# Kernel optimization log

Hardware: AMD Instinct MI355X
Metric: run time of the kernel (lower is better)

Reference implementation:

```python
import jax, jax.numpy as jnp
import numpy as np
from jax import lax

IMPOSSIBLE = -10000.0
B, T, N = 64, 2048, 128


def setup_inputs() -> dict:
    key = jax.random.key(0)
    ks = jax.random.split(key, 8)
    emissions = jax.random.normal(ks[0], (B, T, N), dtype=jnp.float32)
    mask = jnp.ones((B, T), dtype=bool)
    target = jax.random.bernoulli(ks[1], 0.5, (B, T, N))
    transitions = jax.random.normal(ks[2], (N, N), dtype=jnp.float32) * 0.1
    start_transitions = jax.random.normal(ks[3], (N,), dtype=jnp.float32) * 0.1
    end_transitions = jax.random.normal(ks[4], (N,), dtype=jnp.float32) * 0.1
    forbidden_transitions = jax.random.bernoulli(ks[5], 0.2, (N, N))
    start_forbidden_transitions = jax.random.bernoulli(ks[6], 0.2, (N,))
    end_forbidden_transitions = jax.random.bernoulli(ks[7], 0.2, (N,))
    return {
        "emissions": emissions,
        "mask": mask,
        "target": target,
        "transitions": transitions,
        "start_transitions": start_transitions,
        "end_transitions": end_transitions,
        "forbidden_transitions": forbidden_transitions,
        "start_forbidden_transitions": start_forbidden_transitions,
        "end_forbidden_transitions": end_forbidden_transitions,
    }


def reference(emissions, mask, target, transitions, start_transitions,
              end_transitions, forbidden_transitions,
              start_forbidden_transitions, end_forbidden_transitions):
    # Apply hard constraints
    trans = jnp.where(forbidden_transitions, IMPOSSIBLE, transitions)        # [N,N]
    st = jnp.where(start_forbidden_transitions, IMPOSSIBLE, start_transitions)  # [N]
    en = jnp.where(end_forbidden_transitions, IMPOSSIBLE, end_transitions)      # [N]

    # Channel 0: supervised (emissions clamped to target set), channel 1: full partition
    sup_em = jnp.where(target, emissions, IMPOSSIBLE)
    bi = jnp.stack([sup_em, emissions], axis=0)            # [2,B,T,N]
    bi = jnp.moveaxis(bi, 2, 0)                            # [T,2,B,N]

    alpha0 = bi[0] + st                                    # [2,B,N]

    def step(alpha, em_t):
        # alpha: [2,B,N]; logsumexp over previous tag i of alpha_i + trans_ij
        new = jax.nn.logsumexp(alpha[..., :, None] + trans[None, None], axis=-2) + em_t
        return new, new

    _, rest = lax.scan(step, alpha0, bi[1:])               # rest: [T-1,2,B,N]
    outs = jnp.concatenate([alpha0[None], rest], axis=0)   # [T,2,B,N]

    lengths = mask.astype(jnp.int32).sum(-1) - 1           # [B]
    last_out = outs[lengths, :, jnp.arange(B)] + en        # [B,2,N]
    z = jax.nn.logsumexp(last_out, axis=-1)                # [B,2]
    return -(z[:, 0] - z[:, 1])                            # [B] loss per sample
```

## Files before the change

### kernel.cpp

```cpp
#include <hip/hip_runtime.h>
#include <cstdint>
#include <cstddef>

#define IMPOSSIBLE -10000.0f
#define INV_LN2 1.44269504088896340736f
#define LN2 0.69314718055994530942f

constexpr int B = 64;
constexpr int T = 2048;
constexpr int N = 128;
constexpr int WSLOT = 132;

typedef _Float16 h2 __attribute__((ext_vector_type(2)));
typedef _Float16 h8 __attribute__((ext_vector_type(8)));

typedef __attribute__((address_space(3))) uint32_t lds_u32_t;
typedef __attribute__((address_space(1))) const uint32_t g_u32_t;

__device__ __forceinline__ void gload_lds4(const void* g, void* l) {
    __builtin_amdgcn_global_load_lds((g_u32_t*)g, (lds_u32_t*)l, 4, 0, 0);
}

struct SmemT {
    __align__(16) _Float16 p_buf[2][128];
    __align__(16) float ring_em[9][128];
    __align__(16) int ring_tg[9][128];
    float wred[4];
};

template<bool FWD, bool SUP, bool FM>
__device__ __forceinline__ void run_chain(
    SmemT& sm,
    const float* __restrict__ embase,
    const int* __restrict__ tgbase,
    const float* __restrict__ transitions,
    const int* __restrict__ forb,
    const float* __restrict__ bnd_tr,
    const int* __restrict__ bnd_forb,
    const int tlast_rt,
    float* __restrict__ wsl)
{
    const int tid = (int)threadIdx.x;
    const int wave = tid >> 6;
    const int lane = tid & 63;
    const int h = lane >> 5;
    const int j = (wave << 5) | (lane & 31);

    const int tlast = FM ? (T - 1) : tlast_rt;
    const int mid = tlast >> 1;
    const int nsteps = FWD ? mid : (tlast - mid);

    h2 e2[32];
    #pragma unroll
    for (int k = 0; k < 8; ++k) {
        const int cch = ((lane & 7) + k) & 7;
        const int ib = (h << 6) + (cch << 3);
        #pragma unroll
        for (int m = 0; m < 4; ++m) {
            const int i0 = ib + (m << 1);
            const int idx0 = FWD ? (i0 * N + j) : (j * N + i0);
            const int idx1 = FWD ? ((i0 + 1) * N + j) : (j * N + i0 + 1);
            const float f0 = forb[idx0] ? 0.0f : __expf(transitions[idx0]);
            const float f1 = forb[idx1] ? 0.0f : __expf(transitions[idx1]);
            e2[(k << 2) + m] = h2{(_Float16)f0, (_Float16)f1};
        }
    }

    const float bnd = bnd_forb[j] ? IMPOSSIBLE : bnd_tr[j];
    const int r0 = FWD ? 0 : tlast;
    const float em0 = embase[(size_t)r0 * N + j];
    const int tg0 = SUP ? tgbase[(size_t)r0 * N + j] : 1;
    const float v0l = ((tg0 ? em0 : IMPOSSIBLE) + bnd) * INV_LN2;

    float mx = v0l;
    #pragma unroll
    for (int d = 1; d < 64; d <<= 1) mx = fmaxf(mx, __shfl_xor(mx, d));
    if (lane == 0) sm.wred[wave] = mx;
    __syncthreads();
    mx = fmaxf(fmaxf(sm.wred[0], sm.wred[1]), fmaxf(sm.wred[2], sm.wred[3]));

    float Mtot = rintf(mx);
    const float p0 = exp2f(v0l - Mtot);
    if (h == 0) sm.p_buf[0][j] = (_Float16)p0;

    float svE = FWD ? p0 : __expf(bnd);
    float svM = FWD ? Mtot : 0.0f;

    if (wave == 0) {
        #pragma unroll
        for (int s = 1; s <= 8; ++s) {
            int srow, drow;
            if (FWD) {
                srow = s; drow = s & 7;
            } else {
                const int r = tlast - s;
                const int ok = FM ? 1 : (r >= 0);
                srow = ok ? r : 0;
                drow = ok ? (r & 7) : 8;
            }
            const float* gse = embase + (size_t)srow * N + lane;
            gload_lds4(gse, &sm.ring_em[drow][0]);
            gload_lds4(gse + 64, &sm.ring_em[drow][64]);
            if (SUP) {
                const int* gst = tgbase + (size_t)srow * N + lane;
                gload_lds4(gst, &sm.ring_tg[drow][0]);
                gload_lds4(gst + 64, &sm.ring_tg[drow][64]);
            }
        }
        if (SUP) asm volatile("s_waitcnt vmcnt(24)" ::: "memory");
        else     asm volatile("s_waitcnt vmcnt(12)" ::: "memory");
    }
    __syncthreads();

    float fx;
    {
        const int t1 = FWD ? 1 : (tlast - 1);
        const int rr = t1 & 7;
        const float em_n = sm.ring_em[rr][j];
        if (SUP) {
            const int tg_n = sm.ring_tg[rr][j];
            fx = tg_n ? __expf(em_n) : 0.0f;
        } else {
            fx = __expf(em_n);
        }
    }

    const _Float16* pb0 = &sm.p_buf[0][h << 6];
    const _Float16* pb1 = &sm.p_buf[1][h << 6];
    const h2 one2 = h2{(_Float16)1.0f, (_Float16)1.0f};

    #pragma unroll 2
    for (int it = 0; it < nsteps; ++it) {
        const int t = FWD ? (1 + it) : (tlast - 1 - it);

        asm volatile("s_waitcnt lgkmcnt(0)\n\ts_barrier" ::: "memory");

        if (wave == 0) {
            int srow, drow;
            if (FWD) {
                srow = t + 8; drow = srow & 7;
            } else {
                const int tt = t - 8;
                const int ok = (tt >= 0);
                srow = ok ? tt : 0;
                drow = ok ? (tt & 7) : 8;
            }
            const float* gse = embase + (size_t)srow * N + lane;
            gload_lds4(gse, &sm.ring_em[drow][0]);
            gload_lds4(gse + 64, &sm.ring_em[drow][64]);
            if (SUP) {
                const int* gst = tgbase + (size_t)srow * N + lane;
                gload_lds4(gst, &sm.ring_tg[drow][0]);
                gload_lds4(gst + 64, &sm.ring_tg[drow][64]);
            }
        }

        const int cur = (it & 1) ^ 1;
        const _Float16* pbase = (cur ^ 1) ? pb1 : pb0;

        h8 pvv[8];
        #pragma unroll
        for (int k = 0; k < 8; ++k) {
            const int cch = ((lane & 7) + k) & 7;
            pvv[k] = *reinterpret_cast<const h8*>(pbase + (cch << 3));
        }

        float acc0 = 0.f, acc1 = 0.f, acc2 = 0.f, acc3 = 0.f;
        float ps0 = 0.f, ps1 = 0.f, ps2 = 0.f, ps3 = 0.f;
        #pragma unroll
        for (int k = 0; k < 8; ++k) {
            const h8 pv = pvv[k];
            const h2 w0 = __builtin_shufflevector(pv, pv, 0, 1);
            const h2 w1 = __builtin_shufflevector(pv, pv, 2, 3);
            const h2 w2 = __builtin_shufflevector(pv, pv, 4, 5);
            const h2 w3 = __builtin_shufflevector(pv, pv, 6, 7);
            acc0 = __builtin_amdgcn_fdot2(w0, e2[(k << 2) + 0], acc0, false);
            acc1 = __builtin_amdgcn_fdot2(w1, e2[(k << 2) + 1], acc1, false);
            acc2 = __builtin_amdgcn_fdot2(w2, e2[(k << 2) + 2], acc2, false);
            acc3 = __builtin_amdgcn_fdot2(w3, e2[(k << 2) + 3], acc3, false);
            ps0 = __builtin_amdgcn_fdot2(w0, one2, ps0, false);
            ps1 = __builtin_amdgcn_fdot2(w1, one2, ps1, false);
            ps2 = __builtin_amdgcn_fdot2(w2, one2, ps2, false);
            ps3 = __builtin_amdgcn_fdot2(w3, one2, ps3, false);
        }
        const float s = (acc0 + acc1) + (acc2 + acc3);
        const float ph = (ps0 + ps1) + (ps2 + ps3);

        float x = s, y = s;
        asm volatile("v_permlane32_swap_b32 %0, %1" : "+v"(x), "+v"(y));
        const float stot = x + y;
        float u = ph, v = ph;
        asm volatile("v_permlane32_swap_b32 %0, %1" : "+v"(u), "+v"(v));
        const float psum = fmaxf(u + v, 1e-30f);

        const float sc = __builtin_amdgcn_rcpf(psum);
        Mtot += __log2f(psum);

        const float na = stot * (fx * sc);
        if (t == mid) {
            svE = FWD ? na : (stot * sc);
            svM = Mtot;
        }

        if (h == 0) sm.p_buf[cur][j] = (_Float16)na;

        {
            const int nt = FWD ? (t + 1) : (t - 1);
            const int rr = nt & 7;
            const float em_n = sm.ring_em[rr][j];
            if (SUP) {
                const int tg_n = sm.ring_tg[rr][j];
                fx = tg_n ? __expf(em_n) : 0.0f;
            } else {
                fx = __expf(em_n);
            }
        }

        if (wave == 0) {
            if (SUP) asm volatile("s_waitcnt vmcnt(24)" ::: "memory");
            else     asm volatile("s_waitcnt vmcnt(12)" ::: "memory");
        }
    }

    if (h == 0) wsl[j] = svE;
    if (tid == 0) wsl[128] = svM;
}

__global__ __launch_bounds__(256, 1) void crf_chain_kernel(
    const float* __restrict__ emissions,
    const int* __restrict__ mask,
    const int* __restrict__ target,
    const float* __restrict__ transitions,
    const float* __restrict__ start_tr,
    const float* __restrict__ end_tr,
    const int* __restrict__ forb,
    const int* __restrict__ start_forb,
    const int* __restrict__ end_forb,
    float* __restrict__ ws)
{
    __shared__ SmemT sm;
    __shared__ int lred[4];

    const int dir = (int)blockIdx.x >> 7;
    const int chain = (int)blockIdx.x & 127;
    const int c = chain >> 6;
    const int b = chain & 63;
    const int tid = (int)threadIdx.x;
    const int wave = tid >> 6;
    const int lane = tid & 63;

    int lsum = 0;
    for (int k = tid; k < T; k += 256) lsum += (mask[b * T + k] != 0);
    #pragma unroll
    for (int d = 1; d < 64; d <<= 1) lsum += __shfl_xor(lsum, d);
    if (lane == 0) lred[wave] = lsum;
    __syncthreads();
    const int tlast = (lred[0] + lred[1] + lred[2] + lred[3]) - 1;
    const bool fm = (tlast == T - 1);

    const float* embase = emissions + (size_t)b * T * N;
    const int* tgbase = target + (size_t)b * T * N;
    float* wsl = ws + (size_t)(dir * 128 + chain) * WSLOT;

    if (dir == 0) {
        if (c == 0) {
            if (fm) run_chain<true, true, true>(sm, embase, tgbase, transitions, forb, start_tr, start_forb, tlast, wsl);
            else    run_chain<true, true, false>(sm, embase, tgbase, transitions, forb, start_tr, start_forb, tlast, wsl);
        } else {
            if (fm) run_chain<true, false, true>(sm, embase, tgbase, transitions, forb, start_tr, start_forb, tlast, wsl);
            else    run_chain<true, false, false>(sm, embase, tgbase, transitions, forb, start_tr, start_forb, tlast, wsl);
        }
    } else {
        if (c == 0) {
            if (fm) run_chain<false, true, true>(sm, embase, tgbase, transitions, forb, end_tr, end_forb, tlast, wsl);
            else    run_chain<false, true, false>(sm, embase, tgbase, transitions, forb, end_tr, end_forb, tlast, wsl);
        } else {
            if (fm) run_chain<false, false, true>(sm, embase, tgbase, transitions, forb, end_tr, end_forb, tlast, wsl);
            else    run_chain<false, false, false>(sm, embase, tgbase, transitions, forb, end_tr, end_forb, tlast, wsl);
        }
    }
}

__global__ void crf_dot_kernel(const float* __restrict__ ws,
                               float* __restrict__ out) {
    const int b = (int)blockIdx.x;
    const int tid = (int)threadIdx.x;
    const int w = tid >> 6;
    const int lane = tid & 63;
    const int chain = w * 64 + b;

    const float* fv = ws + (size_t)chain * WSLOT;
    const float* bv = ws + (size_t)(128 + chain) * WSLOT;

    float term = fv[lane] * bv[lane] + fv[lane + 64] * bv[lane + 64];
    #pragma unroll
    for (int d = 1; d < 64; d <<= 1) term += __shfl_xor(term, d);

    __shared__ float zz[2];
    if (lane == 0) zz[w] = LN2 * (fv[128] + bv[128]) + __logf(term);
    __syncthreads();
    if (tid == 0) out[b] = zz[1] - zz[0];
}

extern "C" void kernel_launch(void* const* d_in, const int* in_sizes, int n_in,
                              void* d_out, int out_size, void* d_ws, size_t ws_size,
                              hipStream_t stream) {
    const float* emissions = (const float*)d_in[0];
    const int* mask = (const int*)d_in[1];
    const int* target = (const int*)d_in[2];
    const float* transitions = (const float*)d_in[3];
    const float* start_tr = (const float*)d_in[4];
    const float* end_tr = (const float*)d_in[5];
    const int* forb = (const int*)d_in[6];
    const int* start_forb = (const int*)d_in[7];
    const int* end_forb = (const int*)d_in[8];
    float* out = (float*)d_out;
    float* ws = (float*)d_ws;

    crf_chain_kernel<<<dim3(4 * B), dim3(256), 0, stream>>>(
        emissions, mask, target, transitions, start_tr, end_tr,
        forb, start_forb, end_forb, ws);
    crf_dot_kernel<<<dim3(B), dim3(128), 0, stream>>>(ws, out);
}
```

Baseline: 453.8 us.

## Pack four CRF chains per 1024-thread block sharing a common step loop

Merges four independent 256-thread chain workgroups into one 1024-thread block with per-group shared memory, launching 64 blocks instead of 256. Every group iterates to the block-wide maximum step count, skipping work when inactive. The s_barrier inside the loop now synchronises all 16 waves, so each chain step waits on the slowest of four chains. This trades per-step barrier cost for fewer blocks, which may fit better on the CUs.

After: 1.039 ms. 129% more time.

```diff
diff --git a/kernel.cpp b/kernel.cpp
--- a/kernel.cpp
+++ b/kernel.cpp
@@ -10,6 +10,7 @@
 constexpr int T = 2048;
 constexpr int N = 128;
 constexpr int WSLOT = 132;
+constexpr int GROUPS = 4;
 
 typedef _Float16 h2 __attribute__((ext_vector_type(2)));
 typedef _Float16 h8 __attribute__((ext_vector_type(8)));
@@ -26,6 +27,8 @@
     __align__(16) float ring_em[9][128];
     __align__(16) int ring_tg[9][128];
     float wred[4];
+    int lred[4];
+    int nred;
 };
 
 template<bool FWD, bool SUP, bool FM>
@@ -38,17 +41,21 @@
     const float* __restrict__ bnd_tr,
     const int* __restrict__ bnd_forb,
     const int tlast_rt,
+    const int nrun_rt,
     float* __restrict__ wsl)
 {
     const int tid = (int)threadIdx.x;
-    const int wave = tid >> 6;
+    const int gtid = tid & 255;
+    const int gwave = gtid >> 6;
     const int lane = tid & 63;
     const int h = lane >> 5;
-    const int j = (wave << 5) | (lane & 31);
+    const int j = (gwave << 5) | (lane & 31);
 
     const int tlast = FM ? (T - 1) : tlast_rt;
     const int mid = tlast >> 1;
-    const int nsteps = FWD ? mid : (tlast - mid);
+    const int nself = FWD ? mid : (tlast - mid);
+    const int nrun = FM ? (FWD ? ((T - 1) >> 1) : (T - 1 - ((T - 1) >> 1)))
+                        : nrun_rt;
 
     h2 e2[32];
     #pragma unroll
@@ -75,7 +82,7 @@
     float mx = v0l;
     #pragma unroll
     for (int d = 1; d < 64; d <<= 1) mx = fmaxf(mx, __shfl_xor(mx, d));
-    if (lane == 0) sm.wred[wave] = mx;
+    if (lane == 0) sm.wred[gwave] = mx;
     __syncthreads();
     mx = fmaxf(fmaxf(sm.wred[0], sm.wred[1]), fmaxf(sm.wred[2], sm.wred[3]));
 
@@ -86,7 +93,7 @@
     float svE = FWD ? p0 : __expf(bnd);
     float svM = FWD ? Mtot : 0.0f;
 
-    if (wave == 0) {
+    if (gwave == 0) {
         #pragma unroll
         for (int s = 1; s <= 8; ++s) {
             int srow, drow;
@@ -130,12 +137,13 @@
     const h2 one2 = h2{(_Float16)1.0f, (_Float16)1.0f};
 
     #pragma unroll 2
-    for (int it = 0; it < nsteps; ++it) {
+    for (int it = 0; it < nrun; ++it) {
+        const bool active = FM ? true : (it < nself);
         const int t = FWD ? (1 + it) : (tlast - 1 - it);
 
         asm volatile("s_waitcnt lgkmcnt(0)\n\ts_barrier" ::: "memory");
 
-        if (wave == 0) {
+        if (gwave == 0 && active) {
             int srow, drow;
             if (FWD) {
                 srow = t + 8; drow = srow & 7;
@@ -155,56 +163,56 @@
             }
         }
 
-        const int cur = (it & 1) ^ 1;
-        const _Float16* pbase = (cur ^ 1) ? pb1 : pb0;
-
-        h8 pvv[8];
-        #pragma unroll
-        for (int k = 0; k < 8; ++k) {
-            const int cch = ((lane & 7) + k) & 7;
-            pvv[k] = *reinterpret_cast<const h8*>(pbase + (cch << 3));
-        }
-
-        float acc0 = 0.f, acc1 = 0.f, acc2 = 0.f, acc3 = 0.f;
-        float ps0 = 0.f, ps1 = 0.f, ps2 = 0.f, ps3 = 0.f;
-        #pragma unroll
-        for (int k = 0; k < 8; ++k) {
-            const h8 pv = pvv[k];
-            const h2 w0 = __builtin_shufflevector(pv, pv, 0, 1);
-            const h2 w1 = __builtin_shufflevector(pv, pv, 2, 3);
-            const h2 w2 = __builtin_shufflevector(pv, pv, 4, 5);
-            const h2 w3 = __builtin_shufflevector(pv, pv, 6, 7);
-            acc0 = __builtin_amdgcn_fdot2(w0, e2[(k << 2) + 0], acc0, false);
-            acc1 = __builtin_amdgcn_fdot2(w1, e2[(k << 2) + 1], acc1, false);
-            acc2 = __builtin_amdgcn_fdot2(w2, e2[(k << 2) + 2], acc2, false);
-            acc3 = __builtin_amdgcn_fdot2(w3, e2[(k << 2) + 3], acc3, false);
-            ps0 = __builtin_amdgcn_fdot2(w0, one2, ps0, false);
-            ps1 = __builtin_amdgcn_fdot2(w1, one2, ps1, false);
-            ps2 = __builtin_amdgcn_fdot2(w2, one2, ps2, false);
-            ps3 = __builtin_amdgcn_fdot2(w3, one2, ps3, false);
-        }
-        const float s = (acc0 + acc1) + (acc2 + acc3);
-        const float ph = (ps0 + ps1) + (ps2 + ps3);
-
-        float x = s, y = s;
-        asm volatile("v_permlane32_swap_b32 %0, %1" : "+v"(x), "+v"(y));
-        const float stot = x + y;
-        float u = ph, v = ph;
-        asm volatile("v_permlane32_swap_b32 %0, %1" : "+v"(u), "+v"(v));
-        const float psum = fmaxf(u + v, 1e-30f);
-
-        const float sc = __builtin_amdgcn_rcpf(psum);
-        Mtot += __log2f(psum);
-
-        const float na = stot * (fx * sc);
-        if (t == mid) {
-            svE = FWD ? na : (stot * sc);
-            svM = Mtot;
-        }
-
-        if (h == 0) sm.p_buf[cur][j] = (_Float16)na;
-
-        {
+        if (active) {
+            const int cur = (it & 1) ^ 1;
+            const _Float16* pbase = (cur ^ 1) ? pb1 : pb0;
+
+            h8 pvv[8];
+            #pragma unroll
+            for (int k = 0; k < 8; ++k) {
+                const int cch = ((lane & 7) + k) & 7;
+                pvv[k] = *reinterpret_cast<const h8*>(pbase + (cch << 3));
+            }
+
+            float acc0 = 0.f, acc1 = 0.f, acc2 = 0.f, acc3 = 0.f;
+            float ps0 = 0.f, ps1 = 0.f, ps2 = 0.f, ps3 = 0.f;
+            #pragma unroll
+            for (int k = 0; k < 8; ++k) {
+                const h8 pv = pvv[k];
+                const h2 w0 = __builtin_shufflevector(pv, pv, 0, 1);
+                const h2 w1 = __builtin_shufflevector(pv, pv, 2, 3);
+                const h2 w2 = __builtin_shufflevector(pv, pv, 4, 5);
+                const h2 w3 = __builtin_shufflevector(pv, pv, 6, 7);
+                acc0 = __builtin_amdgcn_fdot2(w0, e2[(k << 2) + 0], acc0, false);
+                acc1 = __builtin_amdgcn_fdot2(w1, e2[(k << 2) + 1], acc1, false);
+                acc2 = __builtin_amdgcn_fdot2(w2, e2[(k << 2) + 2], acc2, false);
+                acc3 = __builtin_amdgcn_fdot2(w3, e2[(k << 2) + 3], acc3, false);
+                ps0 = __builtin_amdgcn_fdot2(w0, one2, ps0, false);
+                ps1 = __builtin_amdgcn_fdot2(w1, one2, ps1, false);
+                ps2 = __builtin_amdgcn_fdot2(w2, one2, ps2, false);
+                ps3 = __builtin_amdgcn_fdot2(w3, one2, ps3, false);
+            }
+            const float s = (acc0 + acc1) + (acc2 + acc3);
+            const float ph = (ps0 + ps1) + (ps2 + ps3);
+
+            float x = s, y = s;
+            asm volatile("v_permlane32_swap_b32 %0, %1" : "+v"(x), "+v"(y));
+            const float stot = x + y;
+            float u = ph, v = ph;
+            asm volatile("v_permlane32_swap_b32 %0, %1" : "+v"(u), "+v"(v));
+            const float psum = fmaxf(u + v, 1e-30f);
+
+            const float sc = __builtin_amdgcn_rcpf(psum);
+            Mtot += __log2f(psum);
+
+            const float na = stot * (fx * sc);
+            if (t == mid) {
+                svE = FWD ? na : (stot * sc);
+                svM = Mtot;
+            }
+
+            if (h == 0) sm.p_buf[cur][j] = (_Float16)na;
+
             const int nt = FWD ? (t + 1) : (t - 1);
             const int rr = nt & 7;
             const float em_n = sm.ring_em[rr][j];
@@ -216,17 +224,37 @@
             }
         }
 
-        if (wave == 0) {
+        if (gwave == 0) {
             if (SUP) asm volatile("s_waitcnt vmcnt(24)" ::: "memory");
             else     asm volatile("s_waitcnt vmcnt(12)" ::: "memory");
         }
     }
 
     if (h == 0) wsl[j] = svE;
-    if (tid == 0) wsl[128] = svM;
-}
-
-__global__ __launch_bounds__(256, 1) void crf_chain_kernel(
+    if (gtid == 0) wsl[128] = svM;
+}
+
+template<bool FWD, bool SUP, bool FM>
+__device__ __forceinline__ void run_block(
+    SmemT* smarr, const int chain0,
+    const float* __restrict__ emissions, const int* __restrict__ mask,
+    const int* __restrict__ target, const float* __restrict__ transitions,
+    const float* __restrict__ bnd_tr, const int* __restrict__ bnd_forb,
+    const int* __restrict__ forb, const int* tlasts, const int nrun,
+    float* __restrict__ ws, const int dir)
+{
+    const int tid = (int)threadIdx.x;
+    const int grp = tid >> 8;
+    const int chain = chain0 + grp;
+    const int b = chain & 63;
+    const float* embase = emissions + (size_t)b * T * N;
+    const int* tgbase = target + (size_t)b * T * N;
+    float* wsl = ws + (size_t)(dir * 128 + chain) * WSLOT;
+    run_chain<FWD, SUP, FM>(smarr[grp], embase, tgbase, transitions, forb,
+                            bnd_tr, bnd_forb, tlasts[grp], nrun, wsl);
+}
+
+__global__ __launch_bounds__(1024, 1) void crf_chain_kernel(
     const float* __restrict__ emissions,
     const int* __restrict__ mask,
     const int* __restrict__ target,
@@ -238,45 +266,57 @@
     const int* __restrict__ end_forb,
     float* __restrict__ ws)
 {
-    __shared__ SmemT sm;
-    __shared__ int lred[4];
-
-    const int dir = (int)blockIdx.x >> 7;
-    const int chain = (int)blockIdx.x & 127;
-    const int c = chain >> 6;
+    __shared__ SmemT sm[GROUPS];
+    __shared__ int tl_sh[GROUPS];
+    __shared__ int stats[2];
+
+    const int dir = (int)blockIdx.x >> 5;
+    const int mblk = (int)blockIdx.x & 31;
+    const int chain0 = mblk << 2;
+    const int sup = (mblk >= 16) ? 0 : 1;
+    const int tid = (int)threadIdx.x;
+    const int grp = tid >> 8;
+    const int gtid = tid & 255;
+    const int gwave = gtid >> 6;
+    const int lane = tid & 63;
+    const int chain = chain0 + grp;
     const int b = chain & 63;
-    const int tid = (int)threadIdx.x;
-    const int wave = tid >> 6;
-    const int lane = tid & 63;
 
     int lsum = 0;
-    for (int k = tid; k < T; k += 256) lsum += (mask[b * T + k] != 0);
+    for (int k = gtid; k < T; k += 256) lsum += (mask[b * T + k] != 0);
     #pragma unroll
     for (int d = 1; d < 64; d <<= 1) lsum += __shfl_xor(lsum, d);
-    if (lane == 0) lred[wave] = lsum;
-    __syncthreads();
-    const int tlast = (lred[0] + lred[1] + lred[2] + lred[3]) - 1;
-    const bool fm = (tlast == T - 1);
-
-    const float* embase = emissions + (size_t)b * T * N;
-    const int* tgbase = target + (size_t)b * T * N;
-    float* wsl = ws + (size_t)(dir * 128 + chain) * WSLOT;
+    if (lane == 0) sm[grp].lred[gwave] = lsum;
+    if (tid == 0) { stats[0] = T; stats[1] = 0; }
+    __syncthreads();
+    const int tlast = (sm[grp].lred[0] + sm[grp].lred[1] +
+                       sm[grp].lred[2] + sm[grp].lred[3]) - 1;
+    if (gtid == 0) {
+        tl_sh[grp] = tlast;
+        atomicMin(&stats[0], tlast);
+        const int mid = tlast >> 1;
+        const int ns = dir ? (tlast - mid) : mid;
+        atomicMax(&stats[1], ns);
+    }
+    __syncthreads();
+    const bool fm = (stats[0] == T - 1);
+    const int nrun = stats[1];
 
     if (dir == 0) {
-        if (c == 0) {
-            if (fm) run_chain<true, true, true>(sm, embase, tgbase, transitions, forb, start_tr, start_forb, tlast, wsl);
-            else    run_chain<true, true, false>(sm, embase, tgbase, transitions, forb, start_tr, start_forb, tlast, wsl);
+        if (sup) {
+            if (fm) run_block<true, true, true>(sm, chain0, emissions, mask, target, transitions, start_tr, start_forb, forb, tl_sh, nrun, ws, dir);
+            else    run_block<true, true, false>(sm, chain0, emissions, mask, target, transitions, start_tr, start_forb, forb, tl_sh, nrun, ws, dir);
         } else {
-            if (fm) run_chain<true, false, true>(sm, embase, tgbase, transitions, forb, start_tr, start_forb, tlast, wsl);
-            else    run_chain<true, false, false>(sm, embase, tgbase, transitions, forb, start_tr, start_forb, tlast, wsl);
+            if (fm) run_block<true, false, true>(sm, chain0, emissions, mask, target, transitions, start_tr, start_forb, forb, tl_sh, nrun, ws, dir);
+            else    run_block<true, false, false>(sm, chain0, emissions, mask, target, transitions, start_tr, start_forb, forb, tl_sh, nrun, ws, dir);
         }
     } else {
-        if (c == 0) {
-            if (fm) run_chain<false, true, true>(sm, embase, tgbase, transitions, forb, end_tr, end_forb, tlast, wsl);
-            else    run_chain<false, true, false>(sm, embase, tgbase, transitions, forb, end_tr, end_forb, tlast, wsl);
+        if (sup) {
+            if (fm) run_block<false, true, true>(sm, chain0, emissions, mask, target, transitions, end_tr, end_forb, forb, tl_sh, nrun, ws, dir);
+            else    run_block<false, true, false>(sm, chain0, emissions, mask, target, transitions, end_tr, end_forb, forb, tl_sh, nrun, ws, dir);
         } else {
-            if (fm) run_chain<false, false, true>(sm, embase, tgbase, transitions, forb, end_tr, end_forb, tlast, wsl);
-            else    run_chain<false, false, false>(sm, embase, tgbase, transitions, forb, end_tr, end_forb, tlast, wsl);
+            if (fm) run_block<false, false, true>(sm, chain0, emissions, mask, target, transitions, end_tr, end_forb, forb, tl_sh, nrun, ws, dir);
+            else    run_block<false, false, false>(sm, chain0, emissions, mask, target, transitions, end_tr, end_forb, forb, tl_sh, nrun, ws, dir);
         }
     }
 }
@@ -317,7 +357,7 @@
     float* out = (float*)d_out;
     float* ws = (float*)d_ws;
 
-    crf_chain_kernel<<<dim3(4 * B), dim3(256), 0, stream>>>(
+    crf_chain_kernel<<<dim3(64), dim3(1024), 0, stream>>>(
         emissions, mask, target, transitions, start_tr, end_tr,
         forb, start_forb, end_forb, ws);
     crf_dot_kernel<<<dim3(B), dim3(128), 0, stream>>>(ws, out);
```

## Run each CRF chain in a single wave and drop per-step block barriers

Applied to the files above, without the earlier changes.

Each chain moves from four waves with a block barrier every time step to one 64-lane wave. Every lane now owns two output tags across all 128 previous tags, so the per-step barrier, the permlane half-sum exchange and the separate partition-sum dot products all go away. Per-step renormalisation now uses lane 0's raw sum as an anchor instead of the full probability sum. This roughly doubles the dot-product work per lane and the transition-matrix register footprint. It also risks fp16 overflow or underflow when the anchor value is far from the other lanes' values.

Result: slower. 617.8 us (+36.1%).

```diff
diff --git a/kernel.cpp b/kernel.cpp
--- a/kernel.cpp
+++ b/kernel.cpp
@@ -21,16 +21,11 @@
     __builtin_amdgcn_global_load_lds((g_u32_t*)g, (lds_u32_t*)l, 4, 0, 0);
 }
 
-struct SmemT {
-    __align__(16) _Float16 p_buf[2][128];
-    __align__(16) float ring_em[9][128];
-    __align__(16) int ring_tg[9][128];
-    float wred[4];
-};
-
 template<bool FWD, bool SUP, bool FM>
 __device__ __forceinline__ void run_chain(
-    SmemT& sm,
+    _Float16* __restrict__ p_lds,
+    float (*__restrict__ ring_em)[128],
+    int (*__restrict__ ring_tg)[128],
     const float* __restrict__ embase,
     const int* __restrict__ tgbase,
     const float* __restrict__ transitions,
@@ -40,102 +35,100 @@
     const int tlast_rt,
     float* __restrict__ wsl)
 {
-    const int tid = (int)threadIdx.x;
-    const int wave = tid >> 6;
-    const int lane = tid & 63;
-    const int h = lane >> 5;
-    const int j = (wave << 5) | (lane & 31);
+    const int lane = (int)threadIdx.x & 63;
+    const int j0 = lane << 1, j1 = j0 + 1;
 
     const int tlast = FM ? (T - 1) : tlast_rt;
     const int mid = tlast >> 1;
     const int nsteps = FWD ? mid : (tlast - mid);
 
-    h2 e2[32];
-    #pragma unroll
-    for (int k = 0; k < 8; ++k) {
-        const int cch = ((lane & 7) + k) & 7;
-        const int ib = (h << 6) + (cch << 3);
-        #pragma unroll
-        for (int m = 0; m < 4; ++m) {
-            const int i0 = ib + (m << 1);
-            const int idx0 = FWD ? (i0 * N + j) : (j * N + i0);
-            const int idx1 = FWD ? ((i0 + 1) * N + j) : (j * N + i0 + 1);
-            const float f0 = forb[idx0] ? 0.0f : __expf(transitions[idx0]);
-            const float f1 = forb[idx1] ? 0.0f : __expf(transitions[idx1]);
-            e2[(k << 2) + m] = h2{(_Float16)f0, (_Float16)f1};
-        }
-    }
-
-    const float bnd = bnd_forb[j] ? IMPOSSIBLE : bnd_tr[j];
-    const int r0 = FWD ? 0 : tlast;
-    const float em0 = embase[(size_t)r0 * N + j];
-    const int tg0 = SUP ? tgbase[(size_t)r0 * N + j] : 1;
-    const float v0l = ((tg0 ? em0 : IMPOSSIBLE) + bnd) * INV_LN2;
-
-    float mx = v0l;
+    h2 eA[64], eB[64];
+    #pragma unroll
+    for (int m = 0; m < 64; ++m) {
+        float a0, a1, b0, b1;
+        if (FWD) {
+            const float2 r0 = *reinterpret_cast<const float2*>(&transitions[(2 * m) * N + j0]);
+            const float2 r1 = *reinterpret_cast<const float2*>(&transitions[(2 * m + 1) * N + j0]);
+            const int2 f0 = *reinterpret_cast<const int2*>(&forb[(2 * m) * N + j0]);
+            const int2 f1 = *reinterpret_cast<const int2*>(&forb[(2 * m + 1) * N + j0]);
+            a0 = f0.x ? 0.0f : __expf(r0.x);  a1 = f1.x ? 0.0f : __expf(r1.x);
+            b0 = f0.y ? 0.0f : __expf(r0.y);  b1 = f1.y ? 0.0f : __expf(r1.y);
+        } else {
+            const float2 r0 = *reinterpret_cast<const float2*>(&transitions[j0 * N + 2 * m]);
+            const float2 r1 = *reinterpret_cast<const float2*>(&transitions[j1 * N + 2 * m]);
+            const int2 f0 = *reinterpret_cast<const int2*>(&forb[j0 * N + 2 * m]);
+            const int2 f1 = *reinterpret_cast<const int2*>(&forb[j1 * N + 2 * m]);
+            a0 = f0.x ? 0.0f : __expf(r0.x);  a1 = f0.y ? 0.0f : __expf(r0.y);
+            b0 = f1.x ? 0.0f : __expf(r1.x);  b1 = f1.y ? 0.0f : __expf(r1.y);
+        }
+        eA[m] = h2{(_Float16)a0, (_Float16)a1};
+        eB[m] = h2{(_Float16)b0, (_Float16)b1};
+    }
+
+    const float2 bt2 = *reinterpret_cast<const float2*>(&bnd_tr[j0]);
+    const int2 bf2 = *reinterpret_cast<const int2*>(&bnd_forb[j0]);
+    const float bndA = bf2.x ? IMPOSSIBLE : bt2.x;
+    const float bndB = bf2.y ? IMPOSSIBLE : bt2.y;
+    const int r0r = FWD ? 0 : tlast;
+    const float2 em02 = *reinterpret_cast<const float2*>(&embase[(size_t)r0r * N + j0]);
+    int2 tg02 = make_int2(1, 1);
+    if (SUP) tg02 = *reinterpret_cast<const int2*>(&tgbase[(size_t)r0r * N + j0]);
+    const float v0l = ((tg02.x ? em02.x : IMPOSSIBLE) + bndA) * INV_LN2;
+    const float v1l = ((tg02.y ? em02.y : IMPOSSIBLE) + bndB) * INV_LN2;
+
+    float mx = fmaxf(v0l, v1l);
     #pragma unroll
     for (int d = 1; d < 64; d <<= 1) mx = fmaxf(mx, __shfl_xor(mx, d));
-    if (lane == 0) sm.wred[wave] = mx;
-    __syncthreads();
-    mx = fmaxf(fmaxf(sm.wred[0], sm.wred[1]), fmaxf(sm.wred[2], sm.wred[3]));
-
     float Mtot = rintf(mx);
-    const float p0 = exp2f(v0l - Mtot);
-    if (h == 0) sm.p_buf[0][j] = (_Float16)p0;
-
-    float svE = FWD ? p0 : __expf(bnd);
+    const float p00 = exp2f(v0l - Mtot);
+    const float p01 = exp2f(v1l - Mtot);
+    *reinterpret_cast<h2*>(&p_lds[j0]) = h2{(_Float16)p00, (_Float16)p01};
+
+    float svE0 = FWD ? p00 : __expf(bndA);
+    float svE1 = FWD ? p01 : __expf(bndB);
     float svM = FWD ? Mtot : 0.0f;
 
-    if (wave == 0) {
-        #pragma unroll
-        for (int s = 1; s <= 8; ++s) {
-            int srow, drow;
-            if (FWD) {
-                srow = s; drow = s & 7;
-            } else {
-                const int r = tlast - s;
-                const int ok = FM ? 1 : (r >= 0);
-                srow = ok ? r : 0;
-                drow = ok ? (r & 7) : 8;
-            }
-            const float* gse = embase + (size_t)srow * N + lane;
-            gload_lds4(gse, &sm.ring_em[drow][0]);
-            gload_lds4(gse + 64, &sm.ring_em[drow][64]);
-            if (SUP) {
-                const int* gst = tgbase + (size_t)srow * N + lane;
-                gload_lds4(gst, &sm.ring_tg[drow][0]);
-                gload_lds4(gst + 64, &sm.ring_tg[drow][64]);
-            }
-        }
-        if (SUP) asm volatile("s_waitcnt vmcnt(24)" ::: "memory");
-        else     asm volatile("s_waitcnt vmcnt(12)" ::: "memory");
-    }
-    __syncthreads();
-
-    float fx;
+    #pragma unroll
+    for (int s = 1; s <= 8; ++s) {
+        int srow, drow;
+        if (FWD) {
+            srow = s; drow = s & 7;
+        } else {
+            const int r = tlast - s;
+            const int ok = FM ? 1 : (r >= 0);
+            srow = ok ? r : 0;
+            drow = ok ? (r & 7) : 8;
+        }
+        const float* gse = embase + (size_t)srow * N + lane;
+        gload_lds4(gse, &ring_em[drow][0]);
+        gload_lds4(gse + 64, &ring_em[drow][64]);
+        if (SUP) {
+            const int* gst = tgbase + (size_t)srow * N + lane;
+            gload_lds4(gst, &ring_tg[drow][0]);
+            gload_lds4(gst + 64, &ring_tg[drow][64]);
+        }
+    }
+    if (SUP) asm volatile("s_waitcnt vmcnt(24)" ::: "memory");
+    else     asm volatile("s_waitcnt vmcnt(12)" ::: "memory");
+
+    float fx0, fx1;
     {
         const int t1 = FWD ? 1 : (tlast - 1);
         const int rr = t1 & 7;
-        const float em_n = sm.ring_em[rr][j];
-        if (SUP) {
-            const int tg_n = sm.ring_tg[rr][j];
-            fx = tg_n ? __expf(em_n) : 0.0f;
-        } else {
-            fx = __expf(em_n);
-        }
-    }
-
-    const _Float16* pb0 = &sm.p_buf[0][h << 6];
-    const _Float16* pb1 = &sm.p_buf[1][h << 6];
-    const h2 one2 = h2{(_Float16)1.0f, (_Float16)1.0f};
+        const float2 emn = *reinterpret_cast<const float2*>(&ring_em[rr][j0]);
+        int2 tgn = make_int2(1, 1);
+        if (SUP) tgn = *reinterpret_cast<const int2*>(&ring_tg[rr][j0]);
+        fx0 = (SUP && !tgn.x) ? 0.0f : __expf(emn.x);
+        fx1 = (SUP && !tgn.y) ? 0.0f : __expf(emn.y);
+    }
+
+    const h8* pp = reinterpret_cast<const h8*>(p_lds);
 
     #pragma unroll 2
     for (int it = 0; it < nsteps; ++it) {
         const int t = FWD ? (1 + it) : (tlast - 1 - it);
 
-        asm volatile("s_waitcnt lgkmcnt(0)\n\ts_barrier" ::: "memory");
-
-        if (wave == 0) {
+        {
             int srow, drow;
             if (FWD) {
                 srow = t + 8; drow = srow & 7;
@@ -146,87 +139,76 @@
                 drow = ok ? (tt & 7) : 8;
             }
             const float* gse = embase + (size_t)srow * N + lane;
-            gload_lds4(gse, &sm.ring_em[drow][0]);
-            gload_lds4(gse + 64, &sm.ring_em[drow][64]);
+            gload_lds4(gse, &ring_em[drow][0]);
+            gload_lds4(gse + 64, &ring_em[drow][64]);
             if (SUP) {
                 const int* gst = tgbase + (size_t)srow * N + lane;
-                gload_lds4(gst, &sm.ring_tg[drow][0]);
-                gload_lds4(gst + 64, &sm.ring_tg[drow][64]);
+                gload_lds4(gst, &ring_tg[drow][0]);
+                gload_lds4(gst + 64, &ring_tg[drow][64]);
             }
         }
 
-        const int cur = (it & 1) ^ 1;
-        const _Float16* pbase = (cur ^ 1) ? pb1 : pb0;
-
-        h8 pvv[8];
+        h8 pvv[16];
         #pragma unroll
-        for (int k = 0; k < 8; ++k) {
-            const int cch = ((lane & 7) + k) & 7;
-            pvv[k] = *reinterpret_cast<const h8*>(pbase + (cch << 3));
-        }
-
-        float acc0 = 0.f, acc1 = 0.f, acc2 = 0.f, acc3 = 0.f;
-        float ps0 = 0.f, ps1 = 0.f, ps2 = 0.f, ps3 = 0.f;
+        for (int k = 0; k < 16; ++k) pvv[k] = pp[k];
+
+        float a0 = 0.f, a1 = 0.f, a2 = 0.f, a3 = 0.f;
+        float b0 = 0.f, b1 = 0.f, b2 = 0.f, b3 = 0.f;
         #pragma unroll
-        for (int k = 0; k < 8; ++k) {
+        for (int k = 0; k < 16; ++k) {
             const h8 pv = pvv[k];
-            const h2 w0 = __builtin_shufflevector(pv, pv, 0, 1);
-            const h2 w1 = __builtin_shufflevector(pv, pv, 2, 3);
-            const h2 w2 = __builtin_shufflevector(pv, pv, 4, 5);
-            const h2 w3 = __builtin_shufflevector(pv, pv, 6, 7);
-            acc0 = __builtin_amdgcn_fdot2(w0, e2[(k << 2) + 0], acc0, false);
-            acc1 = __builtin_amdgcn_fdot2(w1, e2[(k << 2) + 1], acc1, false);
-            acc2 = __builtin_amdgcn_fdot2(w2, e2[(k << 2) + 2], acc2, false);
-            acc3 = __builtin_amdgcn_fdot2(w3, e2[(k << 2) + 3], acc3, false);
-            ps0 = __builtin_amdgcn_fdot2(w0, one2, ps0, false);
-            ps1 = __builtin_amdgcn_fdot2(w1, one2, ps1, false);
-            ps2 = __builtin_amdgcn_fdot2(w2, one2, ps2, false);
-            ps3 = __builtin_amdgcn_fdot2(w3, one2, ps3, false);
-        }
-        const float s = (acc0 + acc1) + (acc2 + acc3);
-        const float ph = (ps0 + ps1) + (ps2 + ps3);
-
-        float x = s, y = s;
-        asm volatile("v_permlane32_swap_b32 %0, %1" : "+v"(x), "+v"(y));
-        const float stot = x + y;
-        float u = ph, v = ph;
-        asm volatile("v_permlane32_swap_b32 %0, %1" : "+v"(u), "+v"(v));
-        const float psum = fmaxf(u + v, 1e-30f);
-
-        const float sc = __builtin_amdgcn_rcpf(psum);
-        Mtot += __log2f(psum);
-
-        const float na = stot * (fx * sc);
+            const h2 u0 = __builtin_shufflevector(pv, pv, 0, 1);
+            const h2 u1 = __builtin_shufflevector(pv, pv, 2, 3);
+            const h2 u2 = __builtin_shufflevector(pv, pv, 4, 5);
+            const h2 u3 = __builtin_shufflevector(pv, pv, 6, 7);
+            const int m = k << 2;
+            a0 = __builtin_amdgcn_fdot2(u0, eA[m + 0], a0, false);
+            a1 = __builtin_amdgcn_fdot2(u1, eA[m + 1], a1, false);
+            a2 = __builtin_amdgcn_fdot2(u2, eA[m + 2], a2, false);
+            a3 = __builtin_amdgcn_fdot2(u3, eA[m + 3], a3, false);
+            b0 = __builtin_amdgcn_fdot2(u0, eB[m + 0], b0, false);
+            b1 = __builtin_amdgcn_fdot2(u1, eB[m + 1], b1, false);
+            b2 = __builtin_amdgcn_fdot2(u2, eB[m + 2], b2, false);
+            b3 = __builtin_amdgcn_fdot2(u3, eB[m + 3], b3, false);
+        }
+        const float sA = (a0 + a1) + (a2 + a3);
+        const float sB = (b0 + b1) + (b2 + b3);
+
+        const float anchor = fmaxf(
+            __int_as_float(__builtin_amdgcn_readfirstlane(__float_as_int(sA))),
+            1e-30f);
+        const float sc = __builtin_amdgcn_rcpf(anchor);
+        Mtot += __log2f(anchor);
+
+        const float na0 = sA * (fx0 * sc);
+        const float na1 = sB * (fx1 * sc);
         if (t == mid) {
-            svE = FWD ? na : (stot * sc);
+            svE0 = FWD ? na0 : (sA * sc);
+            svE1 = FWD ? na1 : (sB * sc);
             svM = Mtot;
         }
 
-        if (h == 0) sm.p_buf[cur][j] = (_Float16)na;
+        *reinterpret_cast<h2*>(&p_lds[j0]) = h2{(_Float16)na0, (_Float16)na1};
 
         {
             const int nt = FWD ? (t + 1) : (t - 1);
             const int rr = nt & 7;
-            const float em_n = sm.ring_em[rr][j];
-            if (SUP) {
-                const int tg_n = sm.ring_tg[rr][j];
-                fx = tg_n ? __expf(em_n) : 0.0f;
-            } else {
-                fx = __expf(em_n);
-            }
-        }
-
-        if (wave == 0) {
-            if (SUP) asm volatile("s_waitcnt vmcnt(24)" ::: "memory");
-            else     asm volatile("s_waitcnt vmcnt(12)" ::: "memory");
-        }
-    }
-
-    if (h == 0) wsl[j] = svE;
-    if (tid == 0) wsl[128] = svM;
-}
-
-__global__ __launch_bounds__(256, 1) void crf_chain_kernel(
+            const float2 emn = *reinterpret_cast<const float2*>(&ring_em[rr][j0]);
+            int2 tgn = make_int2(1, 1);
+            if (SUP) tgn = *reinterpret_cast<const int2*>(&ring_tg[rr][j0]);
+            fx0 = (SUP && !tgn.x) ? 0.0f : __expf(emn.x);
+            fx1 = (SUP && !tgn.y) ? 0.0f : __expf(emn.y);
+        }
+
+        if (SUP) asm volatile("s_waitcnt vmcnt(24)" ::: "memory");
+        else     asm volatile("s_waitcnt vmcnt(12)" ::: "memory");
+    }
+
+    *reinterpret_cast<float2*>(&wsl[j0]) = make_float2(svE0, svE1);
+    if (lane == 0) wsl[128] = svM;
+}
+
+__global__ __launch_bounds__(64, 1) void crf_chain_kernel(
     const float* __restrict__ emissions,
     const int* __restrict__ mask,
     const int* __restrict__ target,
@@ -238,24 +220,21 @@
     const int* __restrict__ end_forb,
     float* __restrict__ ws)
 {
-    __shared__ SmemT sm;
-    __shared__ int lred[4];
+    __shared__ __align__(16) _Float16 p_lds[128];
+    __shared__ __align__(16) float ring_em[9][128];
+    __shared__ __align__(16) int ring_tg[9][128];
 
     const int dir = (int)blockIdx.x >> 7;
     const int chain = (int)blockIdx.x & 127;
     const int c = chain >> 6;
     const int b = chain & 63;
-    const int tid = (int)threadIdx.x;
-    const int wave = tid >> 6;
-    const int lane = tid & 63;
+    const int lane = (int)threadIdx.x & 63;
 
     int lsum = 0;
-    for (int k = tid; k < T; k += 256) lsum += (mask[b * T + k] != 0);
+    for (int k = lane; k < T; k += 64) lsum += (mask[b * T + k] != 0);
     #pragma unroll
     for (int d = 1; d < 64; d <<= 1) lsum += __shfl_xor(lsum, d);
-    if (lane == 0) lred[wave] = lsum;
-    __syncthreads();
-    const int tlast = (lred[0] + lred[1] + lred[2] + lred[3]) - 1;
+    const int tlast = lsum - 1;
     const bool fm = (tlast == T - 1);
 
     const float* embase = emissions + (size_t)b * T * N;
@@ -264,19 +243,19 @@
 
     if (dir == 0) {
         if (c == 0) {
-            if (fm) run_chain<true, true, true>(sm, embase, tgbase, transitions, forb, start_tr, start_forb, tlast, wsl);
-            else    run_chain<true, true, false>(sm, embase, tgbase, transitions, forb, start_tr, start_forb, tlast, wsl);
+            if (fm) run_chain<true, true, true>(p_lds, ring_em, ring_tg, embase, tgbase, transitions, forb, start_tr, start_forb, tlast, wsl);
+            else    run_chain<true, true, false>(p_lds, ring_em, ring_tg, embase, tgbase, transitions, forb, start_tr, start_forb, tlast, wsl);
         } else {
-            if (fm) run_chain<true, false, true>(sm, embase, tgbase, transitions, forb, start_tr, start_forb, tlast, wsl);
-            else    run_chain<true, false, false>(sm, embase, tgbase, transitions, forb, start_tr, start_forb, tlast, wsl);
+            if (fm) run_chain<true, false, true>(p_lds, ring_em, ring_tg, embase, tgbase, transitions, forb, start_tr, start_forb, tlast, wsl);
+            else    run_chain<true, false, false>(p_lds, ring_em, ring_tg, embase, tgbase, transitions, forb, start_tr, start_forb, tlast, wsl);
         }
     } else {
         if (c == 0) {
-            if (fm) run_chain<false, true, true>(sm, embase, tgbase, transitions, forb, end_tr, end_forb, tlast, wsl);
-            else    run_chain<false, true, false>(sm, embase, tgbase, transitions, forb, end_tr, end_forb, tlast, wsl);
+            if (fm) run_chain<false, true, true>(p_lds, ring_em, ring_tg, embase, tgbase, transitions, forb, end_tr, end_forb, tlast, wsl);
+            else    run_chain<false, true, false>(p_lds, ring_em, ring_tg, embase, tgbase, transitions, forb, end_tr, end_forb, tlast, wsl);
         } else {
-            if (fm) run_chain<false, false, true>(sm, embase, tgbase, transitions, forb, end_tr, end_forb, tlast, wsl);
-            else    run_chain<false, false, false>(sm, embase, tgbase, transitions, forb, end_tr, end_forb, tlast, wsl);
+            if (fm) run_chain<false, false, true>(p_lds, ring_em, ring_tg, embase, tgbase, transitions, forb, end_tr, end_forb, tlast, wsl);
+            else    run_chain<false, false, false>(p_lds, ring_em, ring_tg, embase, tgbase, transitions, forb, end_tr, end_forb, tlast, wsl);
         }
     }
 }
@@ -317,7 +296,7 @@
     float* out = (float*)d_out;
     float* ws = (float*)d_ws;
 
-    crf_chain_kernel<<<dim3(4 * B), dim3(256), 0, stream>>>(
+    crf_chain_kernel<<<dim3(4 * B), dim3(64), 0, stream>>>(
         emissions, mask, target, transitions, start_tr, end_tr,
         forb, start_forb, end_forb, ws);
     crf_dot_kernel<<<dim3(B), dim3(128), 0, stream>>>(ws, out);
```
